# Kernel tuning notes

Hardware: AMD Instinct MI355X
Metric: run time of the kernel (lower is better)

The kernel has to match this reference:

```python
import jax, jax.numpy as jnp
from jax import lax
import numpy as np

N_ASSETS = 128
BATCH = 2048
MAX_WEIGHT = 1.0
N_ITERS = 300      # projected-gradient iterations (unrolled solver)
N_BISECT = 40      # bisection steps for simplex-box projection
LR = 0.02
EPS = 1e-8


def project_capped_simplex(v, c):
    """Project rows of v onto {w : sum(w)=1, -c <= w <= c} via bisection on the
    shift tau in w = clip(v - tau, -c, c). sum is decreasing in tau."""
    lo = jnp.min(v, axis=-1, keepdims=True) - c - 1.0
    hi = jnp.max(v, axis=-1, keepdims=True) + c

    def body(carry, _):
        lo, hi = carry
        mid = 0.5 * (lo + hi)
        s = jnp.sum(jnp.clip(v - mid, -c, c), axis=-1, keepdims=True)
        too_big = s > 1.0
        return (jnp.where(too_big, mid, lo), jnp.where(too_big, hi, mid)), None

    (lo, hi), _ = lax.scan(body, (lo, hi), None, length=N_BISECT)
    tau = 0.5 * (lo + hi)
    return jnp.clip(v - tau, -c, c)


def solve_markowitz(rets, A, alpha_abs, max_weight):
    """maximize r.w - sqrt(w'Aw) - alpha*||w||_2  s.t. sum w = 1, |w| <= c,
    via projected gradient ascent (fixed iteration count, fully batched)."""
    B, n = rets.shape
    w0 = jnp.full((B, n), 1.0 / n, dtype=rets.dtype)
    a = alpha_abs[:, None]

    def step(w, _):
        Aw = jnp.einsum('bij,bj->bi', A, w)                       # (B,n)
        risk = jnp.sqrt(jnp.sum(w * Aw, axis=-1, keepdims=True) + EPS)
        nrm = jnp.sqrt(jnp.sum(w * w, axis=-1, keepdims=True) + EPS)
        g = rets - Aw / risk - a * (w / nrm)                      # gradient of objective
        w_new = project_capped_simplex(w + LR * g, max_weight)
        return w_new, None

    w, _ = lax.scan(step, w0, None, length=N_ITERS)
    return w


def setup_inputs() -> dict:
    key = jax.random.key(0)
    k1, k2, k3, k4 = jax.random.split(key, 4)
    rets = 0.05 * jax.random.normal(k1, (BATCH, N_ASSETS), dtype=jnp.float32)
    # PSD covariance: B B^T / n + jitter*I
    Bm = jax.random.normal(k2, (BATCH, N_ASSETS, N_ASSETS), dtype=jnp.float32)
    covmat = jnp.einsum('bik,bjk->bij', Bm, Bm) / N_ASSETS
    covmat = covmat + 1e-3 * jnp.eye(N_ASSETS, dtype=jnp.float32)
    gamma = jax.random.uniform(k3, (BATCH,), dtype=jnp.float32, minval=0.1, maxval=2.0)
    alpha = jax.random.normal(k4, (BATCH,), dtype=jnp.float32)
    return {"rets": rets, "covmat": covmat, "gamma": gamma, "alpha": alpha}


def reference(rets, covmat, gamma, alpha):
    alpha_abs = jnp.abs(alpha)
    A = gamma[:, None, None] * covmat   # gamma-adjusted covariance, as in forward
    return solve_markowitz(rets, A, alpha_abs, MAX_WEIGHT)
```

## Files before the change

### kernel.cpp

```cpp
#include <hip/hip_runtime.h>
#include <math.h>

#define NA      128
#define NBATCH  2048
#define NTHR    512
#define NIT     300
#define NBIS    40
#define LRC     0.02f
#define EPSC    1e-8f

template <int CTRL>
__device__ __forceinline__ float dpp_sum_step(float x) {
  int s = __builtin_amdgcn_update_dpp(0, __float_as_int(x), CTRL, 0xF, 0xF, true);
  return x + __int_as_float(s);
}
__device__ __forceinline__ float wave_sum64(float x) {
  x = dpp_sum_step<0x111>(x);
  x = dpp_sum_step<0x112>(x);
  x = dpp_sum_step<0x114>(x);
  x = dpp_sum_step<0x118>(x);
  x = dpp_sum_step<0x142>(x);
  x = dpp_sum_step<0x143>(x);
  return x;
}
template <int CTRL>
__device__ __forceinline__ float dpp_mov_self(float x) {
  int s = __builtin_amdgcn_update_dpp(__float_as_int(x), __float_as_int(x), CTRL, 0xF, 0xF, false);
  return __int_as_float(s);
}
__device__ __forceinline__ float wave_min64(float x) {
  x = fminf(x, dpp_mov_self<0x111>(x));
  x = fminf(x, dpp_mov_self<0x112>(x));
  x = fminf(x, dpp_mov_self<0x114>(x));
  x = fminf(x, dpp_mov_self<0x118>(x));
  x = fminf(x, dpp_mov_self<0x142>(x));
  x = fminf(x, dpp_mov_self<0x143>(x));
  return x;
}
__device__ __forceinline__ float wave_max64(float x) {
  x = fmaxf(x, dpp_mov_self<0x111>(x));
  x = fmaxf(x, dpp_mov_self<0x112>(x));
  x = fmaxf(x, dpp_mov_self<0x114>(x));
  x = fmaxf(x, dpp_mov_self<0x118>(x));
  x = fmaxf(x, dpp_mov_self<0x142>(x));
  x = fmaxf(x, dpp_mov_self<0x143>(x));
  return x;
}
__device__ __forceinline__ float bcast63(float x) {
  return __int_as_float(__builtin_amdgcn_readlane(__float_as_int(x), 63));
}
__device__ __forceinline__ float clip1(float x) {
  return __builtin_amdgcn_fmed3f(x, -1.0f, 1.0f);
}

__global__ __launch_bounds__(NTHR)
void markowitz_kernel(
    const float* __restrict__ rets,
    const float* __restrict__ covmat,
    const float* __restrict__ gamma,
    const float* __restrict__ alpha,
    float* __restrict__ out)
{
  const int b    = blockIdx.x;
  const int tid  = threadIdx.x;
  const int r    = tid & (NA - 1);
  const int q    = tid >> 7;
  const int lane = tid & 63;
  const int wv   = tid >> 6;
  const int chain_wv = b & 7;

  __shared__ __align__(16) float ws[NA];
  __shared__ __align__(16) float vs[NA];
  __shared__ __align__(16) float part[NTHR];
  __shared__ float pp[4];

  const float gm = gamma[b];
  const float4* Aq = reinterpret_cast<const float4*>(
      covmat + (size_t)b * NA * NA + (size_t)r * NA + (size_t)q * 32);
  float4 a[8];
#pragma unroll
  for (int k = 0; k < 8; ++k) {
    float4 t = Aq[k];
    a[k] = make_float4(t.x * gm, t.y * gm, t.z * gm, t.w * gm);
  }
  const float av = fabsf(alpha[b]);
  float r_c = 0.0f;
  if (tid < NA) { r_c = rets[b * NA + tid]; ws[tid] = 1.0f / NA; }
  __syncthreads();

#pragma unroll 1
  for (int it = 0; it < NIT; ++it) {
    const float4* w4 = reinterpret_cast<const float4*>(ws) + q * 8;
    float4 acc = make_float4(0.f, 0.f, 0.f, 0.f);
#pragma unroll
    for (int k = 0; k < 8; ++k) {
      float4 wk = w4[k];
      acc.x = fmaf(a[k].x, wk.x, acc.x);
      acc.y = fmaf(a[k].y, wk.y, acc.y);
      acc.z = fmaf(a[k].z, wk.z, acc.z);
      acc.w = fmaf(a[k].w, wk.w, acc.w);
    }
    part[tid] = (acc.x + acc.y) + (acc.z + acc.w);
    __syncthreads();

    float Aw = 0.f, w_c = 0.f, v_c = 0.f;
    if (tid < NA) {
      Aw  = (part[tid] + part[tid + NA]) + (part[tid + 2 * NA] + part[tid + 3 * NA]);
      w_c = ws[tid];
      float p1 = wave_sum64(w_c * Aw);
      float p2 = wave_sum64(w_c * w_c);
      if (lane == 63) { pp[wv * 2 + 0] = p1; pp[wv * 2 + 1] = p2; }
    }
    __syncthreads();

    if (tid < NA) {
      const float risk = sqrtf(pp[0] + pp[2] + EPSC);
      const float nrm  = sqrtf(pp[1] + pp[3] + EPSC);
      const float g    = r_c - Aw / risk - av * (w_c / nrm);
      v_c = w_c + LRC * g;
      vs[tid] = v_c;
    }
    __syncthreads();

    if (wv == chain_wv) {
      float v0 = vs[lane];
      float v1 = vs[lane + 64];
      float mn = bcast63(wave_min64(fminf(v0, v1)));
      float mx = bcast63(wave_max64(fmaxf(v0, v1)));
      float lo = mn - 2.0f;
      float hi = mx + 1.0f;
#pragma unroll 1
      for (int rr = 0; rr < NBIS; ++rr) {
        const float mid = 0.5f * (lo + hi);
        float s = wave_sum64(clip1(v0 - mid) + clip1(v1 - mid));
        const float st = bcast63(s);
        const bool big = st > 1.0f;
        lo = big ? mid : lo;
        hi = big ? hi : mid;
      }
      const float tau = 0.5f * (lo + hi);
      ws[lane]      = clip1(v0 - tau);
      ws[lane + 64] = clip1(v1 - tau);
    }
    __syncthreads();
  }

  if (tid < NA) out[b * NA + tid] = ws[tid];
}

extern "C" void kernel_launch(void* const* d_in, const int* in_sizes, int n_in,
                              void* d_out, int out_size, void* d_ws, size_t ws_size,
                              hipStream_t stream) {
  const float* rets   = (const float*)d_in[0];
  const float* covmat = (const float*)d_in[1];
  const float* gamma  = (const float*)d_in[2];
  const float* alpha  = (const float*)d_in[3];
  float* out = (float*)d_out;

  hipLaunchKernelGGL(markowitz_kernel, dim3(NBATCH), dim3(NTHR), 0, stream,
                     rets, covmat, gamma, alpha, out);
}
```

Measured before the change: 2.685 ms.

## Halve block size, keep covariance rows in AGPRs, fold gradient into single wave

The block shrinks from 512 to 256 threads. Each thread now holds 64 gamma-scaled covariance values, parked in accumulator registers through inline asm and read back each iteration for the matvec. The gradient, norm and risk computation moves into the single chain wave alongside the bisection, which removes two block barriers per iteration and the vs/pp shared buffers. The bisection also exits early once lo/hi stop changing. The cost is more per-thread matvec work and an AGPR read before every FMA, and the hand-pinned asm register names may constrain the compiler's scheduling.

```diff
diff --git a/kernel.cpp b/kernel.cpp
--- a/kernel.cpp
+++ b/kernel.cpp
@@ -3,7 +3,7 @@
 
 #define NA      128
 #define NBATCH  2048
-#define NTHR    512
+#define NTHR    256
 #define NIT     300
 #define NBIS    40
 #define LRC     0.02f
@@ -53,6 +53,19 @@
   return __builtin_amdgcn_fmed3f(x, -1.0f, 1.0f);
 }
 
+#define AW2(R, X) asm volatile("v_accvgpr_write_b32 a" #R ", %0" :: "v"(X) : "a" #R)
+#define AW(R, X)  AW2(R, X)
+#define AR2(R, D) asm volatile("v_accvgpr_read_b32 %0, a" #R : "=v"(D) : : "a" #R)
+#define AR(R, D)  AR2(R, D)
+
+#define STAGE(K, R0, R1, R2, R3) do { float4 qq = Ar[K]; \
+  AW(R0, qq.x * gm); AW(R1, qq.y * gm); AW(R2, qq.z * gm); AW(R3, qq.w * gm); } while (0)
+
+#define DOT(K, R0, R1, R2, R3) do { const float4 wk = w4[K]; float x0, x1, x2, x3; \
+  AR(R0, x0); AR(R1, x1); AR(R2, x2); AR(R3, x3); \
+  acc.x = fmaf(x0, wk.x, acc.x); acc.y = fmaf(x1, wk.y, acc.y); \
+  acc.z = fmaf(x2, wk.z, acc.z); acc.w = fmaf(x3, wk.w, acc.w); } while (0)
+
 __global__ __launch_bounds__(NTHR)
 void markowitz_kernel(
     const float* __restrict__ rets,
@@ -61,86 +74,79 @@
     const float* __restrict__ alpha,
     float* __restrict__ out)
 {
-  const int b    = blockIdx.x;
-  const int tid  = threadIdx.x;
-  const int r    = tid & (NA - 1);
-  const int q    = tid >> 7;
-  const int lane = tid & 63;
-  const int wv   = tid >> 6;
-  const int chain_wv = b & 7;
+  const int b     = blockIdx.x;
+  const int tid   = threadIdx.x;
+  const int r     = tid & (NA - 1);
+  const int h     = tid >> 7;
+  const int lane  = tid & 63;
+  const int wv    = tid >> 6;
+  const int chain = b & 3;
 
   __shared__ __align__(16) float ws[NA];
-  __shared__ __align__(16) float vs[NA];
   __shared__ __align__(16) float part[NTHR];
-  __shared__ float pp[4];
 
   const float gm = gamma[b];
-  const float4* Aq = reinterpret_cast<const float4*>(
-      covmat + (size_t)b * NA * NA + (size_t)r * NA + (size_t)q * 32);
-  float4 a[8];
-#pragma unroll
-  for (int k = 0; k < 8; ++k) {
-    float4 t = Aq[k];
-    a[k] = make_float4(t.x * gm, t.y * gm, t.z * gm, t.w * gm);
-  }
+  const float4* Ar = reinterpret_cast<const float4*>(
+      covmat + (size_t)b * NA * NA + (size_t)r * NA + (size_t)h * 64);
+  STAGE( 0,  0,  1,  2,  3);  STAGE( 1,  4,  5,  6,  7);
+  STAGE( 2,  8,  9, 10, 11);  STAGE( 3, 12, 13, 14, 15);
+  STAGE( 4, 16, 17, 18, 19);  STAGE( 5, 20, 21, 22, 23);
+  STAGE( 6, 24, 25, 26, 27);  STAGE( 7, 28, 29, 30, 31);
+  STAGE( 8, 32, 33, 34, 35);  STAGE( 9, 36, 37, 38, 39);
+  STAGE(10, 40, 41, 42, 43);  STAGE(11, 44, 45, 46, 47);
+  STAGE(12, 48, 49, 50, 51);  STAGE(13, 52, 53, 54, 55);
+  STAGE(14, 56, 57, 58, 59);  STAGE(15, 60, 61, 62, 63);
+
   const float av = fabsf(alpha[b]);
-  float r_c = 0.0f;
-  if (tid < NA) { r_c = rets[b * NA + tid]; ws[tid] = 1.0f / NA; }
+  const float rA = rets[b * NA + lane];
+  const float rB = rets[b * NA + lane + 64];
+
+  if (tid < NA) ws[tid] = 1.0f / NA;
   __syncthreads();
 
 #pragma unroll 1
   for (int it = 0; it < NIT; ++it) {
-    const float4* w4 = reinterpret_cast<const float4*>(ws) + q * 8;
+    const float4* w4 = reinterpret_cast<const float4*>(ws) + h * 16;
     float4 acc = make_float4(0.f, 0.f, 0.f, 0.f);
-#pragma unroll
-    for (int k = 0; k < 8; ++k) {
-      float4 wk = w4[k];
-      acc.x = fmaf(a[k].x, wk.x, acc.x);
-      acc.y = fmaf(a[k].y, wk.y, acc.y);
-      acc.z = fmaf(a[k].z, wk.z, acc.z);
-      acc.w = fmaf(a[k].w, wk.w, acc.w);
-    }
+    DOT( 0,  0,  1,  2,  3);  DOT( 1,  4,  5,  6,  7);
+    DOT( 2,  8,  9, 10, 11);  DOT( 3, 12, 13, 14, 15);
+    DOT( 4, 16, 17, 18, 19);  DOT( 5, 20, 21, 22, 23);
+    DOT( 6, 24, 25, 26, 27);  DOT( 7, 28, 29, 30, 31);
+    DOT( 8, 32, 33, 34, 35);  DOT( 9, 36, 37, 38, 39);
+    DOT(10, 40, 41, 42, 43);  DOT(11, 44, 45, 46, 47);
+    DOT(12, 48, 49, 50, 51);  DOT(13, 52, 53, 54, 55);
+    DOT(14, 56, 57, 58, 59);  DOT(15, 60, 61, 62, 63);
     part[tid] = (acc.x + acc.y) + (acc.z + acc.w);
     __syncthreads();
 
-    float Aw = 0.f, w_c = 0.f, v_c = 0.f;
-    if (tid < NA) {
-      Aw  = (part[tid] + part[tid + NA]) + (part[tid + 2 * NA] + part[tid + 3 * NA]);
-      w_c = ws[tid];
-      float p1 = wave_sum64(w_c * Aw);
-      float p2 = wave_sum64(w_c * w_c);
-      if (lane == 63) { pp[wv * 2 + 0] = p1; pp[wv * 2 + 1] = p2; }
-    }
-    __syncthreads();
-
-    if (tid < NA) {
-      const float risk = sqrtf(pp[0] + pp[2] + EPSC);
-      const float nrm  = sqrtf(pp[1] + pp[3] + EPSC);
-      const float g    = r_c - Aw / risk - av * (w_c / nrm);
-      v_c = w_c + LRC * g;
-      vs[tid] = v_c;
-    }
-    __syncthreads();
-
-    if (wv == chain_wv) {
-      float v0 = vs[lane];
-      float v1 = vs[lane + 64];
-      float mn = bcast63(wave_min64(fminf(v0, v1)));
-      float mx = bcast63(wave_max64(fmaxf(v0, v1)));
+    if (wv == chain) {
+      const float AwA = part[lane] + part[lane + 128];
+      const float AwB = part[lane + 64] + part[lane + 192];
+      const float wA  = ws[lane];
+      const float wB  = ws[lane + 64];
+      const float risk = sqrtf(bcast63(wave_sum64(wA * AwA + wB * AwB)) + EPSC);
+      const float nrm  = sqrtf(bcast63(wave_sum64(wA * wA + wB * wB)) + EPSC);
+      const float gA = rA - AwA / risk - av * (wA / nrm);
+      const float gB = rB - AwB / risk - av * (wB / nrm);
+      const float vA = wA + LRC * gA;
+      const float vB = wB + LRC * gB;
+      const float mn = bcast63(wave_min64(fminf(vA, vB)));
+      const float mx = bcast63(wave_max64(fmaxf(vA, vB)));
       float lo = mn - 2.0f;
       float hi = mx + 1.0f;
 #pragma unroll 1
       for (int rr = 0; rr < NBIS; ++rr) {
         const float mid = 0.5f * (lo + hi);
-        float s = wave_sum64(clip1(v0 - mid) + clip1(v1 - mid));
-        const float st = bcast63(s);
-        const bool big = st > 1.0f;
-        lo = big ? mid : lo;
-        hi = big ? hi : mid;
+        const float st  = bcast63(wave_sum64(clip1(vA - mid) + clip1(vB - mid)));
+        const bool  big = st > 1.0f;
+        const float nlo = big ? mid : lo;
+        const float nhi = big ? hi : mid;
+        if (nlo == lo && nhi == hi) break;
+        lo = nlo; hi = nhi;
       }
       const float tau = 0.5f * (lo + hi);
-      ws[lane]      = clip1(v0 - tau);
-      ws[lane + 64] = clip1(v1 - tau);
+      ws[lane]      = clip1(vA - tau);
+      ws[lane + 64] = clip1(vB - tau);
     }
     __syncthreads();
   }
```

Result: slower. 3.354 ms (+24.9%).
